# Performance work log

Measured on AMD Instinct MI355X. Metric: run time of the kernel, lower is better.

## Reference

```python
import jax, jax.numpy as jnp
import numpy as np

N = 100000
E = 1600000
IN_C = 128
HID = 32
OUT_C = 32
HEADS = 4
NEG_SLOPE = 0.2


def setup_inputs() -> dict:
    key = jax.random.key(0)
    ks = jax.random.split(key, 8)
    x = jax.random.normal(ks[0], (N, IN_C), dtype=jnp.float32)
    edge_index = jax.random.randint(ks[1], (2, E), 0, N, dtype=jnp.int64)
    s = 0.1
    W1 = jax.random.normal(ks[2], (IN_C, HEADS * HID), dtype=jnp.float32) * s
    att_src1 = jax.random.normal(ks[3], (HEADS, HID), dtype=jnp.float32) * s
    att_dst1 = jax.random.normal(ks[4], (HEADS, HID), dtype=jnp.float32) * s
    W2 = jax.random.normal(ks[5], (HEADS * HID, HEADS * OUT_C), dtype=jnp.float32) * s
    att_src2 = jax.random.normal(ks[6], (HEADS, OUT_C), dtype=jnp.float32) * s
    att_dst2 = jax.random.normal(ks[7], (HEADS, OUT_C), dtype=jnp.float32) * s
    return {"x": x, "edge_index": edge_index, "W1": W1, "att_src1": att_src1,
            "att_dst1": att_dst1, "W2": W2, "att_src2": att_src2, "att_dst2": att_dst2}


def _gat_conv(x, src, dst, W, a_src, a_dst, heads, ch):
    # linear transform: [N, heads, ch]
    h = (x @ W).reshape(-1, heads, ch)
    # per-node attention logits [N, heads]
    al_src = jnp.sum(h * a_src, axis=-1)
    al_dst = jnp.sum(h * a_dst, axis=-1)
    # per-edge attention [E, heads]
    e = jax.nn.leaky_relu(al_src[src] + al_dst[dst], negative_slope=NEG_SLOPE)
    # segment softmax over incoming edges of each dst node
    m = jax.ops.segment_max(e, dst, num_segments=N)
    e = jnp.exp(e - m[dst])
    denom = jax.ops.segment_sum(e, dst, num_segments=N)
    alpha = e / (denom[dst] + 1e-16)
    # message + scatter-add aggregation
    msg = h[src] * alpha[:, :, None]          # [E, heads, ch]
    out = jax.ops.segment_sum(msg, dst, num_segments=N)
    return out.reshape(-1, heads * ch)        # concat heads (PyG default)


def reference(x, edge_index, W1, att_src1, att_dst1, W2, att_src2, att_dst2):
    # add self-loops (PyG GATConv default add_self_loops=True)
    loop = jnp.arange(N, dtype=edge_index.dtype)
    src = jnp.concatenate([edge_index[0], loop])
    dst = jnp.concatenate([edge_index[1], loop])
    h = _gat_conv(x, src, dst, W1, att_src1, att_dst1, HEADS, HID)
    h = jax.nn.relu(h)  # dropout is identity in eval mode
    out = _gat_conv(h, src, dst, W2, att_src2, att_dst2, HEADS, OUT_C)
    return out
```

## Files before the change

### kernel.cpp

```cpp
#include <hip/hip_runtime.h>

#define NN 100000
#define EE 1600000
#define NGRP 8
#define DRANGE 12500
#define SLOTS 72
#define NROWPAD 100032
#define NTILES 1563

typedef short bf16x8 __attribute__((ext_vector_type(8)));
typedef float f32x4 __attribute__((ext_vector_type(4)));

__device__ __forceinline__ float leaky(float x) { return x > 0.f ? x : 0.2f * x; }

__device__ __forceinline__ unsigned int bfpack2(float a, float b)
{
    unsigned int xa = __float_as_uint(a), xb = __float_as_uint(b);
    xa = (xa + 0x7fffu + ((xa >> 16) & 1u)) >> 16;
    xb = (xb + 0x7fffu + ((xb >> 16) & 1u)) & 0xffff0000u;
    return xa | xb;
}

__device__ __forceinline__ unsigned short bf1(float a)
{
    unsigned int x = __float_as_uint(a);
    return (unsigned short)((x + 0x7fffu + ((x >> 16) & 1u)) >> 16);
}

__device__ __forceinline__ float blo(unsigned int u) { return __uint_as_float(u << 16); }
__device__ __forceinline__ float bhi(unsigned int u) { return __uint_as_float(u & 0xffff0000u); }


__global__ __launch_bounds__(256) void prep_x(const float* __restrict__ X,
                                              unsigned int* __restrict__ Xbf)
{
    const int tid0 = blockIdx.x * 256 + threadIdx.x;
    const int nthr = gridDim.x * 256;
    const int total = NROWPAD * 16;
    for (int i = tid0; i < total; i += nthr) {
        int row = i >> 4, inner = i & 15;
        uint4 o;
        if (row < NN) {
            const float* p = X + (size_t)row * 128 + inner * 8;
            float4 f0 = *(const float4*)p;
            float4 f1 = *(const float4*)(p + 4);
            o.x = bfpack2(f0.x, f0.y); o.y = bfpack2(f0.z, f0.w);
            o.z = bfpack2(f1.x, f1.y); o.w = bfpack2(f1.z, f1.w);
        } else {
            o = make_uint4(0, 0, 0, 0);
        }
        *(uint4*)&Xbf[(size_t)i * 4] = o;
    }
}

__global__ __launch_bounds__(256) void prep_w(const float* __restrict__ W1, const float* __restrict__ W2,
                                              unsigned short* __restrict__ Wtb1, unsigned short* __restrict__ Wtb2)
{
    int tid = blockIdx.x * 256 + threadIdx.x;
    int layer = tid >> 12;
    int rem = tid & 4095;
    int c = rem >> 5;
    int kq = (rem & 31) * 4;
    const float* Ws = layer ? W2 : W1;
    unsigned short* Wd = layer ? Wtb2 : Wtb1;
    ushort4 o;
    o.x = bf1(Ws[(kq + 0) * 128 + c]);
    o.y = bf1(Ws[(kq + 1) * 128 + c]);
    o.z = bf1(Ws[(kq + 2) * 128 + c]);
    o.w = bf1(Ws[(kq + 3) * 128 + c]);
    *(ushort4*)&Wd[c * 128 + kq] = o;
}


__global__ __launch_bounds__(256) void build_kernel(const int* __restrict__ src, const int* __restrict__ dst,
                                                    int* __restrict__ cnt, int* __restrict__ csr)
{
    const int grp = blockIdx.x & (NGRP - 1);
    const int gr  = blockIdx.x >> 3;
    const int ng  = gridDim.x >> 3;
    const int dlo = grp * DRANGE, dhi = dlo + DRANGE;
    const int tid0 = gr * 256 + threadIdx.x;
    const int nthr = ng * 256;
    for (int e4 = tid0 * 4; e4 < EE; e4 += nthr * 4) {
        int4 dv = *(const int4*)&dst[e4];
        int4 sv = *(const int4*)&src[e4];
        #pragma unroll
        for (int j = 0; j < 4; ++j) {
            int d = (&dv.x)[j];
            if (d >= dlo && d < dhi) {
                int pos = atomicAdd(&cnt[d], 1);
                if (pos < SLOTS) csr[(size_t)d * SLOTS + pos] = (&sv.x)[j];
            }
        }
    }
}


__global__ __launch_bounds__(256) void gemm_mfma(const unsigned short* __restrict__ Xbf,
                                                 const unsigned short* __restrict__ Wtb,
                                                 const float* __restrict__ att_src,
                                                 const float* __restrict__ att_dst,
                                                 unsigned int* __restrict__ Hbf,
                                                 float* __restrict__ alS, float* __restrict__ alD)
{
    const int w = threadIdx.x >> 6, lane = threadIdx.x & 63;
    const int cl = lane & 15, b = lane >> 4;

    bf16x8 Bf[8][4];
    #pragma unroll
    for (int c = 0; c < 8; c++)
        #pragma unroll
        for (int s = 0; s < 4; s++)
            Bf[c][s] = *(const bf16x8*)(Wtb + (16 * c + cl) * 128 + 32 * s + 8 * b);

    float asv[8], adv[8];
    #pragma unroll
    for (int c = 0; c < 8; c++) { asv[c] = att_src[16 * c + cl]; adv[c] = att_dst[16 * c + cl]; }

    for (int tile = blockIdx.x; tile < NTILES; tile += gridDim.x) {
        const int rowb = tile * 64 + 16 * w;
        const unsigned short* pa = Xbf + (size_t)(rowb + cl) * 128 + 8 * b;
        bf16x8 Af[4];
        #pragma unroll
        for (int s = 0; s < 4; s++) Af[s] = *(const bf16x8*)(pa + 32 * s);

        f32x4 acc[8];
        #pragma unroll
        for (int c = 0; c < 8; c++) acc[c] = (f32x4){0.f, 0.f, 0.f, 0.f};
        #pragma unroll
        for (int s = 0; s < 4; s++)
            #pragma unroll
            for (int c = 0; c < 8; c++)
                acc[c] = __builtin_amdgcn_mfma_f32_16x16x32_bf16(Af[s], Bf[c][s], acc[c], 0, 0, 0);

        const int row0 = rowb + 4 * b;
        #pragma unroll
        for (int c = 0; c < 8; c++) {
            #pragma unroll
            for (int r = 0; r < 4; r++) {
                float partner = __shfl_xor(acc[c][r], 1);
                if (!(cl & 1) && row0 + r < NN)
                    Hbf[(size_t)(row0 + r) * 64 + 8 * c + (cl >> 1)] = bfpack2(acc[c][r], partner);
            }
        }
        #pragma unroll
        for (int r = 0; r < 4; r++) {
            float ps0 = 0, ps1 = 0, ps2 = 0, ps3 = 0;
            float pd0 = 0, pd1 = 0, pd2 = 0, pd3 = 0;
            #pragma unroll
            for (int c = 0; c < 8; c++) {
                float v = acc[c][r];
                if (c < 2)      { ps0 += v * asv[c]; pd0 += v * adv[c]; }
                else if (c < 4) { ps1 += v * asv[c]; pd1 += v * adv[c]; }
                else if (c < 6) { ps2 += v * asv[c]; pd2 += v * adv[c]; }
                else            { ps3 += v * asv[c]; pd3 += v * adv[c]; }
            }
            float t0 = ps0 + __shfl_xor(ps0, 1);
            float t1 = ps1 + __shfl_xor(ps1, 1);
            float t2 = ps2 + __shfl_xor(ps2, 1);
            float t3 = ps3 + __shfl_xor(ps3, 1);
            float a0 = (cl & 1) ? t1 : t0;
            float a1 = (cl & 1) ? t3 : t2;
            a0 += __shfl_xor(a0, 2);
            a1 += __shfl_xor(a1, 2);
            float av = (cl & 2) ? a1 : a0;
            av += __shfl_xor(av, 4);
            av += __shfl_xor(av, 8);
            t0 = pd0 + __shfl_xor(pd0, 1);
            t1 = pd1 + __shfl_xor(pd1, 1);
            t2 = pd2 + __shfl_xor(pd2, 1);
            t3 = pd3 + __shfl_xor(pd3, 1);
            a0 = (cl & 1) ? t1 : t0;
            a1 = (cl & 1) ? t3 : t2;
            a0 += __shfl_xor(a0, 2);
            a1 += __shfl_xor(a1, 2);
            float dv = (cl & 2) ? a1 : a0;
            dv += __shfl_xor(dv, 4);
            dv += __shfl_xor(dv, 8);
            if (cl < 4 && row0 + r < NN) {
                alS[(row0 + r) * 4 + cl] = av;
                alD[(row0 + r) * 4 + cl] = dv;
            }
        }
    }
}


__global__ __launch_bounds__(256) void agg_kernel(const unsigned int* __restrict__ Hbf,
                                                  const int* __restrict__ cnt, const int* __restrict__ csr,
                                                  const float* __restrict__ alS, const float* __restrict__ alD,
                                                  float* __restrict__ OUTf, unsigned int* __restrict__ OUTb,
                                                  int do_relu)
{
    __shared__ float pl[4][64 * 4];
    __shared__ int   sl[4][64];
    const int w = threadIdx.x >> 6, lane = threadIdx.x & 63;
    const int wid = (blockIdx.x * 256 + threadIdx.x) >> 6;
    if (wid >= NN) return;
    const int nreal = min(cnt[wid], SLOTS);
    const int nE = nreal + 1;
    const float4 ad = *(const float4*)&alD[wid * 4];
    const int half = lane >> 5, l5 = lane & 31;
    const int hq = l5 >> 3;
    const uint2* __restrict__ H2 = (const uint2*)Hbf + l5;
    const int* __restrict__ slots = csr + (size_t)wid * SLOTS;

    float4 acc = make_float4(0.f, 0.f, 0.f, 0.f);
    float den = 0.f;
    for (int base = 0; base < nE; base += 64) {
        const int nthis = min(64, nE - base);
        const int idx = base + lane;
        int s_ = 0;
        float4 p = make_float4(0.f, 0.f, 0.f, 0.f);
        if (lane < nthis) {
            s_ = (idx == nreal) ? wid : slots[idx];
            float4 as = *(const float4*)&alS[s_ * 4];
            p.x = __expf(leaky(as.x + ad.x));
            p.y = __expf(leaky(as.y + ad.y));
            p.z = __expf(leaky(as.z + ad.z));
            p.w = __expf(leaky(as.w + ad.w));
        }
        sl[w][lane] = s_;
        *(float4*)&pl[w][lane * 4] = p;
        int k = 0;
        for (; k + 8 <= nthis; k += 8) {
            float p0 = pl[w][(k + half) * 4 + hq];
            float p1 = pl[w][(k + 2 + half) * 4 + hq];
            float p2 = pl[w][(k + 4 + half) * 4 + hq];
            float p3 = pl[w][(k + 6 + half) * 4 + hq];
            int s0i = sl[w][k + half];
            int s1i = sl[w][k + 2 + half];
            int s2i = sl[w][k + 4 + half];
            int s3i = sl[w][k + 6 + half];
            uint2 u0 = H2[(size_t)s0i * 32];
            uint2 u1 = H2[(size_t)s1i * 32];
            uint2 u2 = H2[(size_t)s2i * 32];
            uint2 u3 = H2[(size_t)s3i * 32];
            den += (p0 + p1) + (p2 + p3);
            acc.x += p0 * blo(u0.x); acc.y += p0 * bhi(u0.x);
            acc.z += p0 * blo(u0.y); acc.w += p0 * bhi(u0.y);
            acc.x += p1 * blo(u1.x); acc.y += p1 * bhi(u1.x);
            acc.z += p1 * blo(u1.y); acc.w += p1 * bhi(u1.y);
            acc.x += p2 * blo(u2.x); acc.y += p2 * bhi(u2.x);
            acc.z += p2 * blo(u2.y); acc.w += p2 * bhi(u2.y);
            acc.x += p3 * blo(u3.x); acc.y += p3 * bhi(u3.x);
            acc.z += p3 * blo(u3.y); acc.w += p3 * bhi(u3.y);
        }
        for (; k < nthis; k += 2) {
            float paf = pl[w][(k + half) * 4 + hq];
            int sa = sl[w][k + half];
            uint2 ua = H2[(size_t)sa * 32];
            den += paf;
            acc.x += paf * blo(ua.x); acc.y += paf * bhi(ua.x);
            acc.z += paf * blo(ua.y); acc.w += paf * bhi(ua.y);
        }
    }
    acc.x += __shfl_xor(acc.x, 32);
    acc.y += __shfl_xor(acc.y, 32);
    acc.z += __shfl_xor(acc.z, 32);
    acc.w += __shfl_xor(acc.w, 32);
    den   += __shfl_xor(den,   32);
    if (half == 0) {
        float inv = 1.f / (den + 1e-16f);
        float o0 = acc.x * inv, o1 = acc.y * inv, o2 = acc.z * inv, o3 = acc.w * inv;
        if (do_relu) {
            o0 = fmaxf(o0, 0.f); o1 = fmaxf(o1, 0.f);
            o2 = fmaxf(o2, 0.f); o3 = fmaxf(o3, 0.f);
        }
        if (OUTb) {
            uint2 ov;
            ov.x = bfpack2(o0, o1);
            ov.y = bfpack2(o2, o3);
            *(uint2*)&OUTb[(size_t)wid * 64 + l5 * 2] = ov;
        } else {
            *(float4*)&OUTf[(size_t)wid * 128 + l5 * 4] = make_float4(o0, o1, o2, o3);
        }
    }
}


extern "C" void kernel_launch(void* const* d_in, const int* in_sizes, int n_in,
                              void* d_out, int out_size, void* d_ws, size_t ws_size,
                              hipStream_t stream)
{
    const float* x   = (const float*)d_in[0];
    const int*   ei  = (const int*)d_in[1];
    const float* W1  = (const float*)d_in[2];
    const float* as1 = (const float*)d_in[3];
    const float* ad1 = (const float*)d_in[4];
    const float* W2  = (const float*)d_in[5];
    const float* as2 = (const float*)d_in[6];
    const float* ad2 = (const float*)d_in[7];
    const int* srcp = ei;
    const int* dstp = ei + EE;

    char* w = (char*)d_ws;
    unsigned int* Xbf  = (unsigned int*)w; w += (size_t)NROWPAD * 64 * 4;
    unsigned int* Hbf  = (unsigned int*)w; w += (size_t)NN * 64 * 4;
    unsigned short* Wtb1 = (unsigned short*)w; w += 16384 * 2;
    unsigned short* Wtb2 = (unsigned short*)w; w += 16384 * 2;
    float* alS = (float*)w; w += (size_t)NN * 4 * 4;
    float* alD = (float*)w; w += (size_t)NN * 4 * 4;
    int* cnt    = (int*)w;  w += (size_t)NN * 4;
    int* csr    = (int*)w;  w += (size_t)NN * SLOTS * 4;

    prep_x<<<1024, 256, 0, stream>>>(x, Xbf);
    prep_w<<<32, 256, 0, stream>>>(W1, W2, Wtb1, Wtb2);
    hipMemsetAsync(cnt, 0, NN * sizeof(int), stream);
    build_kernel<<<1568, 256, 0, stream>>>(srcp, dstp, cnt, csr);

    const int node_wave_blocks = (NN + 3) / 4;

    gemm_mfma<<<512, 256, 0, stream>>>((const unsigned short*)Xbf, Wtb1, as1, ad1, Hbf, alS, alD);
    agg_kernel<<<node_wave_blocks, 256, 0, stream>>>(Hbf, cnt, csr, alS, alD, nullptr, Xbf, 1);

    gemm_mfma<<<512, 256, 0, stream>>>((const unsigned short*)Xbf, Wtb2, as2, ad2, Hbf, alS, alD);
    agg_kernel<<<node_wave_blocks, 256, 0, stream>>>(Hbf, cnt, csr, alS, alD, (float*)d_out, nullptr, 0);
}
```

Measured before the change: 291.5 us.

## Fold attention vectors into weights as extra MFMA column; merge prep and build kernels

Precomputes W·a_src and W·a_dst per head as a small bf16 matrix, so the attention logits come from one extra MFMA per k-step instead of a shuffle-reduction epilogue in the GEMM. It also merges prep_x, prep_w, the new attention-weight prep and the CSR build into one launch using block-index ranges, which removes kernel launches and lets the independent work overlap. The logits are now computed from bf16-rounded folded weights rather than fp32 dot products of the GEMM output, which slightly changes numerics.

```diff
diff --git a/kernel.cpp b/kernel.cpp
--- a/kernel.cpp
+++ b/kernel.cpp
@@ -8,6 +8,12 @@
 #define NROWPAD 100032
 #define NTILES 1563
 
+#define PX_BLK 1024
+#define PW_BLK 32
+#define WA_BLK 16
+#define PREP_BLK (PX_BLK + PW_BLK + WA_BLK)
+#define BUILD_BLK 1568
+
 typedef short bf16x8 __attribute__((ext_vector_type(8)));
 typedef float f32x4 __attribute__((ext_vector_type(4)));
 
@@ -31,65 +37,85 @@
 __device__ __forceinline__ float bhi(unsigned int u) { return __uint_as_float(u & 0xffff0000u); }
 
 
-__global__ __launch_bounds__(256) void prep_x(const float* __restrict__ X,
-                                              unsigned int* __restrict__ Xbf)
-{
-    const int tid0 = blockIdx.x * 256 + threadIdx.x;
-    const int nthr = gridDim.x * 256;
-    const int total = NROWPAD * 16;
-    for (int i = tid0; i < total; i += nthr) {
-        int row = i >> 4, inner = i & 15;
-        uint4 o;
-        if (row < NN) {
-            const float* p = X + (size_t)row * 128 + inner * 8;
-            float4 f0 = *(const float4*)p;
-            float4 f1 = *(const float4*)(p + 4);
-            o.x = bfpack2(f0.x, f0.y); o.y = bfpack2(f0.z, f0.w);
-            o.z = bfpack2(f1.x, f1.y); o.w = bfpack2(f1.z, f1.w);
-        } else {
-            o = make_uint4(0, 0, 0, 0);
-        }
-        *(uint4*)&Xbf[(size_t)i * 4] = o;
-    }
-}
-
-__global__ __launch_bounds__(256) void prep_w(const float* __restrict__ W1, const float* __restrict__ W2,
-                                              unsigned short* __restrict__ Wtb1, unsigned short* __restrict__ Wtb2)
-{
-    int tid = blockIdx.x * 256 + threadIdx.x;
-    int layer = tid >> 12;
-    int rem = tid & 4095;
-    int c = rem >> 5;
-    int kq = (rem & 31) * 4;
-    const float* Ws = layer ? W2 : W1;
-    unsigned short* Wd = layer ? Wtb2 : Wtb1;
-    ushort4 o;
-    o.x = bf1(Ws[(kq + 0) * 128 + c]);
-    o.y = bf1(Ws[(kq + 1) * 128 + c]);
-    o.z = bf1(Ws[(kq + 2) * 128 + c]);
-    o.w = bf1(Ws[(kq + 3) * 128 + c]);
-    *(ushort4*)&Wd[c * 128 + kq] = o;
-}
-
-
-__global__ __launch_bounds__(256) void build_kernel(const int* __restrict__ src, const int* __restrict__ dst,
-                                                    int* __restrict__ cnt, int* __restrict__ csr)
-{
-    const int grp = blockIdx.x & (NGRP - 1);
-    const int gr  = blockIdx.x >> 3;
-    const int ng  = gridDim.x >> 3;
-    const int dlo = grp * DRANGE, dhi = dlo + DRANGE;
-    const int tid0 = gr * 256 + threadIdx.x;
-    const int nthr = ng * 256;
-    for (int e4 = tid0 * 4; e4 < EE; e4 += nthr * 4) {
-        int4 dv = *(const int4*)&dst[e4];
-        int4 sv = *(const int4*)&src[e4];
-        #pragma unroll
-        for (int j = 0; j < 4; ++j) {
-            int d = (&dv.x)[j];
-            if (d >= dlo && d < dhi) {
-                int pos = atomicAdd(&cnt[d], 1);
-                if (pos < SLOTS) csr[(size_t)d * SLOTS + pos] = (&sv.x)[j];
+__global__ __launch_bounds__(256) void prep_build(const float* __restrict__ X,
+                                                  unsigned int* __restrict__ Xbf,
+                                                  const float* __restrict__ W1, const float* __restrict__ W2,
+                                                  unsigned short* __restrict__ Wtb1, unsigned short* __restrict__ Wtb2,
+                                                  const float* __restrict__ as1, const float* __restrict__ ad1,
+                                                  const float* __restrict__ as2, const float* __restrict__ ad2,
+                                                  unsigned short* __restrict__ Wa1, unsigned short* __restrict__ Wa2,
+                                                  const int* __restrict__ src, const int* __restrict__ dst,
+                                                  int* __restrict__ cnt, int* __restrict__ csr)
+{
+    const int bid = blockIdx.x;
+    if (bid < PX_BLK) {
+        const int tid0 = bid * 256 + threadIdx.x;
+        const int nthr = PX_BLK * 256;
+        const int total = NROWPAD * 16;
+        for (int i = tid0; i < total; i += nthr) {
+            int row = i >> 4, inner = i & 15;
+            uint4 o;
+            if (row < NN) {
+                const float* p = X + (size_t)row * 128 + inner * 8;
+                float4 f0 = *(const float4*)p;
+                float4 f1 = *(const float4*)(p + 4);
+                o.x = bfpack2(f0.x, f0.y); o.y = bfpack2(f0.z, f0.w);
+                o.z = bfpack2(f1.x, f1.y); o.w = bfpack2(f1.z, f1.w);
+            } else {
+                o = make_uint4(0, 0, 0, 0);
+            }
+            *(uint4*)&Xbf[(size_t)i * 4] = o;
+        }
+    } else if (bid < PX_BLK + PW_BLK) {
+        int tid = (bid - PX_BLK) * 256 + threadIdx.x;
+        int layer = tid >> 12;
+        int rem = tid & 4095;
+        int c = rem >> 5;
+        int kq = (rem & 31) * 4;
+        const float* Ws = layer ? W2 : W1;
+        unsigned short* Wd = layer ? Wtb2 : Wtb1;
+        ushort4 o;
+        o.x = bf1(Ws[(kq + 0) * 128 + c]);
+        o.y = bf1(Ws[(kq + 1) * 128 + c]);
+        o.z = bf1(Ws[(kq + 2) * 128 + c]);
+        o.w = bf1(Ws[(kq + 3) * 128 + c]);
+        *(ushort4*)&Wd[c * 128 + kq] = o;
+    } else if (bid < PREP_BLK) {
+        int tid = (bid - PX_BLK - PW_BLK) * 256 + threadIdx.x;
+        int layer = tid >> 11;
+        int rem = tid & 2047;
+        int col = rem >> 7;
+        int k = rem & 127;
+        const float* Ws = layer ? W2 : W1;
+        unsigned short* Wd = layer ? Wa2 : Wa1;
+        float s = 0.f;
+        if (col < 8) {
+            int head = col & 3;
+            const float* av = (col < 4) ? (layer ? as2 : as1) : (layer ? ad2 : ad1);
+            const float* wr = Ws + k * 128 + head * 32;
+            const float* ar = av + head * 32;
+            #pragma unroll
+            for (int c = 0; c < 32; c++) s += wr[c] * ar[c];
+        }
+        Wd[col * 128 + k] = bf1(s);
+    } else {
+        const int bb = bid - PREP_BLK;
+        const int grp = bb & (NGRP - 1);
+        const int gr  = bb >> 3;
+        const int ng  = BUILD_BLK >> 3;
+        const int dlo = grp * DRANGE, dhi = dlo + DRANGE;
+        const int tid0 = gr * 256 + threadIdx.x;
+        const int nthr = ng * 256;
+        for (int e4 = tid0 * 4; e4 < EE; e4 += nthr * 4) {
+            int4 dv = *(const int4*)&dst[e4];
+            int4 sv = *(const int4*)&src[e4];
+            #pragma unroll
+            for (int j = 0; j < 4; ++j) {
+                int d = (&dv.x)[j];
+                if (d >= dlo && d < dhi) {
+                    int pos = atomicAdd(&cnt[d], 1);
+                    if (pos < SLOTS) csr[(size_t)d * SLOTS + pos] = (&sv.x)[j];
+                }
             }
         }
     }
@@ -98,8 +124,7 @@
 
 __global__ __launch_bounds__(256) void gemm_mfma(const unsigned short* __restrict__ Xbf,
                                                  const unsigned short* __restrict__ Wtb,
-                                                 const float* __restrict__ att_src,
-                                                 const float* __restrict__ att_dst,
+                                                 const unsigned short* __restrict__ Wa,
                                                  unsigned int* __restrict__ Hbf,
                                                  float* __restrict__ alS, float* __restrict__ alD)
 {
@@ -113,9 +138,10 @@
         for (int s = 0; s < 4; s++)
             Bf[c][s] = *(const bf16x8*)(Wtb + (16 * c + cl) * 128 + 32 * s + 8 * b);
 
-    float asv[8], adv[8];
+    bf16x8 Bf9[4];
     #pragma unroll
-    for (int c = 0; c < 8; c++) { asv[c] = att_src[16 * c + cl]; adv[c] = att_dst[16 * c + cl]; }
+    for (int s = 0; s < 4; s++)
+        Bf9[s] = *(const bf16x8*)(Wa + cl * 128 + 32 * s + 8 * b);
 
     for (int tile = blockIdx.x; tile < NTILES; tile += gridDim.x) {
         const int rowb = tile * 64 + 16 * w;
@@ -127,11 +153,14 @@
         f32x4 acc[8];
         #pragma unroll
         for (int c = 0; c < 8; c++) acc[c] = (f32x4){0.f, 0.f, 0.f, 0.f};
-        #pragma unroll
-        for (int s = 0; s < 4; s++)
+        f32x4 acc9 = (f32x4){0.f, 0.f, 0.f, 0.f};
+        #pragma unroll
+        for (int s = 0; s < 4; s++) {
             #pragma unroll
             for (int c = 0; c < 8; c++)
                 acc[c] = __builtin_amdgcn_mfma_f32_16x16x32_bf16(Af[s], Bf[c][s], acc[c], 0, 0, 0);
+            acc9 = __builtin_amdgcn_mfma_f32_16x16x32_bf16(Af[s], Bf9[s], acc9, 0, 0, 0);
+        }
 
         const int row0 = rowb + 4 * b;
         #pragma unroll
@@ -145,41 +174,10 @@
         }
         #pragma unroll
         for (int r = 0; r < 4; r++) {
-            float ps0 = 0, ps1 = 0, ps2 = 0, ps3 = 0;
-            float pd0 = 0, pd1 = 0, pd2 = 0, pd3 = 0;
-            #pragma unroll
-            for (int c = 0; c < 8; c++) {
-                float v = acc[c][r];
-                if (c < 2)      { ps0 += v * asv[c]; pd0 += v * adv[c]; }
-                else if (c < 4) { ps1 += v * asv[c]; pd1 += v * adv[c]; }
-                else if (c < 6) { ps2 += v * asv[c]; pd2 += v * adv[c]; }
-                else            { ps3 += v * asv[c]; pd3 += v * adv[c]; }
-            }
-            float t0 = ps0 + __shfl_xor(ps0, 1);
-            float t1 = ps1 + __shfl_xor(ps1, 1);
-            float t2 = ps2 + __shfl_xor(ps2, 1);
-            float t3 = ps3 + __shfl_xor(ps3, 1);
-            float a0 = (cl & 1) ? t1 : t0;
-            float a1 = (cl & 1) ? t3 : t2;
-            a0 += __shfl_xor(a0, 2);
-            a1 += __shfl_xor(a1, 2);
-            float av = (cl & 2) ? a1 : a0;
-            av += __shfl_xor(av, 4);
-            av += __shfl_xor(av, 8);
-            t0 = pd0 + __shfl_xor(pd0, 1);
-            t1 = pd1 + __shfl_xor(pd1, 1);
-            t2 = pd2 + __shfl_xor(pd2, 1);
-            t3 = pd3 + __shfl_xor(pd3, 1);
-            a0 = (cl & 1) ? t1 : t0;
-            a1 = (cl & 1) ? t3 : t2;
-            a0 += __shfl_xor(a0, 2);
-            a1 += __shfl_xor(a1, 2);
-            float dv = (cl & 2) ? a1 : a0;
-            dv += __shfl_xor(dv, 4);
-            dv += __shfl_xor(dv, 8);
-            if (cl < 4 && row0 + r < NN) {
-                alS[(row0 + r) * 4 + cl] = av;
-                alD[(row0 + r) * 4 + cl] = dv;
+            const int rr = row0 + r;
+            if (rr < NN) {
+                if (cl < 4)      alS[rr * 4 + cl] = acc9[r];
+                else if (cl < 8) alD[rr * 4 + (cl - 4)] = acc9[r];
             }
         }
     }
@@ -299,21 +297,23 @@
     unsigned int* Hbf  = (unsigned int*)w; w += (size_t)NN * 64 * 4;
     unsigned short* Wtb1 = (unsigned short*)w; w += 16384 * 2;
     unsigned short* Wtb2 = (unsigned short*)w; w += 16384 * 2;
+    unsigned short* Wa1  = (unsigned short*)w; w += 2048 * 2;
+    unsigned short* Wa2  = (unsigned short*)w; w += 2048 * 2;
     float* alS = (float*)w; w += (size_t)NN * 4 * 4;
     float* alD = (float*)w; w += (size_t)NN * 4 * 4;
     int* cnt    = (int*)w;  w += (size_t)NN * 4;
     int* csr    = (int*)w;  w += (size_t)NN * SLOTS * 4;
 
-    prep_x<<<1024, 256, 0, stream>>>(x, Xbf);
-    prep_w<<<32, 256, 0, stream>>>(W1, W2, Wtb1, Wtb2);
     hipMemsetAsync(cnt, 0, NN * sizeof(int), stream);
-    build_kernel<<<1568, 256, 0, stream>>>(srcp, dstp, cnt, csr);
+    prep_build<<<PREP_BLK + BUILD_BLK, 256, 0, stream>>>(x, Xbf, W1, W2, Wtb1, Wtb2,
+                                                         as1, ad1, as2, ad2, Wa1, Wa2,
+                                                         srcp, dstp, cnt, csr);
 
     const int node_wave_blocks = (NN + 3) / 4;
 
-    gemm_mfma<<<512, 256, 0, stream>>>((const unsigned short*)Xbf, Wtb1, as1, ad1, Hbf, alS, alD);
+    gemm_mfma<<<512, 256, 0, stream>>>((const unsigned short*)Xbf, Wtb1, Wa1, Hbf, alS, alD);
     agg_kernel<<<node_wave_blocks, 256, 0, stream>>>(Hbf, cnt, csr, alS, alD, nullptr, Xbf, 1);
 
-    gemm_mfma<<<512, 256, 0, stream>>>((const unsigned short*)Xbf, Wtb2, as2, ad2, Hbf, alS, alD);
+    gemm_mfma<<<512, 256, 0, stream>>>((const unsigned short*)Xbf, Wtb2, Wa2, Hbf, alS, alD);
     agg_kernel<<<node_wave_blocks, 256, 0, stream>>>(Hbf, cnt, csr, alS, alD, (float*)d_out, nullptr, 0);
 }
```

New measurement: 284.2 us. -2.5%, faster.
